# Performance work log

Measured on AMD Instinct MI355X. Metric: run time of the kernel, lower is better.

The kernel has to match this reference:

```python
import jax, jax.numpy as jnp
import numpy as np

P = 1024          # nodes per graph
B = 64            # graphs in batch
N = P * B         # total nodes
E = N * 32        # total edges (avg degree 32)
D_IN = 16         # per-node feature dim (share_obs_dim)
H = 32            # GCN / MLP hidden dim (hardcoded in GNet)
SHARE = 64        # flat share_state dim


def setup_inputs() -> dict:
    key = jax.random.key(0)
    ks = jax.random.split(key, 20)

    x = jax.random.normal(ks[0], (N, D_IN), jnp.float32)
    src = jax.random.randint(ks[1], (E,), 0, N, dtype=jnp.int32)
    # keep edges inside each 1024-node graph block (PyG batched graphs)
    dst = (src // P) * P + jax.random.randint(ks[2], (E,), 0, P, dtype=jnp.int32)
    edge_index = jnp.stack([src, dst])
    value_batch = (jnp.arange(N, dtype=jnp.int32) // P)
    share_state = jax.random.normal(ks[3], (B, SHARE), jnp.float32)

    def lin(k, o, i):
        return jax.random.normal(k, (o, i), jnp.float32) / np.float32(np.sqrt(i))

    return {
        "x": x, "edge_index": edge_index, "value_batch": value_batch,
        "share_state": share_state,
        # value_gnet: GCNConv(D_IN,32), GCNConv(32,32), Linear(32,32), post-pool Linear(32,32)
        "W1": lin(ks[4], H, D_IN), "b1": jnp.zeros((H,), jnp.float32),
        "W2": lin(ks[5], H, H),    "b2": jnp.zeros((H,), jnp.float32),
        "Wl": lin(ks[6], H, H),    "bl": jnp.zeros((H,), jnp.float32),
        "Wp": lin(ks[7], H, H),    "bp": jnp.zeros((H,), jnp.float32),
        # value_net MLP: SHARE->32->32->32
        "Vw1": lin(ks[8], H, SHARE), "Vb1": jnp.zeros((H,), jnp.float32),
        "Vw2": lin(ks[9], H, H),     "Vb2": jnp.zeros((H,), jnp.float32),
        "Vw3": lin(ks[10], H, H),    "Vb3": jnp.zeros((H,), jnp.float32),
        # value_comnet: 64->32->1
        "Cw1": lin(ks[11], H, 2 * H), "Cb1": jnp.zeros((H,), jnp.float32),
        "Cw2": lin(ks[12], 1, H) * np.float32(0.01), "Cb2": jnp.zeros((1,), jnp.float32),
    }


def gcn_conv(x, src, dst, W, b):
    """PyG GCNConv: D^-1/2 (A+I) D^-1/2 X W^T + b (unit edge weights)."""
    n = x.shape[0]
    loop = jnp.arange(n, dtype=src.dtype)
    s = jnp.concatenate([src, loop])
    d = jnp.concatenate([dst, loop])
    deg = jax.ops.segment_sum(jnp.ones(s.shape[0], x.dtype), d, num_segments=n)
    dis = jnp.where(deg > 0, jax.lax.rsqrt(jnp.maximum(deg, 1e-12)), 0.0)
    norm = dis[s] * dis[d]                      # [E+N]
    h = x @ W.T                                  # [N, H] small GEMM first
    out = jax.ops.segment_sum(h[s] * norm[:, None], d, num_segments=n)
    return out + b


def reference(x, edge_index, value_batch, share_state,
              W1, b1, W2, b2, Wl, bl, Wp, bp,
              Vw1, Vb1, Vw2, Vb2, Vw3, Vb3,
              Cw1, Cb1, Cw2, Cb2):
    src, dst = edge_index[0], edge_index[1]
    nb = share_state.shape[0]

    # value_gnet
    h = jnp.tanh(gcn_conv(x, src, dst, W1, b1))
    h = jnp.tanh(gcn_conv(h, src, dst, W2, b2))
    h = jnp.tanh(h @ Wl.T + bl)
    pooled = jax.ops.segment_sum(h, value_batch, num_segments=nb)  # global_add_pool -> [B, 32]
    h1 = pooled @ Wp.T + bp

    # value_net MLP on flat share_state
    h2 = jnp.tanh(share_state @ Vw1.T + Vb1)
    h2 = jnp.tanh(h2 @ Vw2.T + Vb2)
    h2 = h2 @ Vw3.T + Vb3

    # value_comnet
    z = jnp.tanh(jnp.concatenate([h1, h2], axis=-1) @ Cw1.T + Cb1)
    value = z @ Cw2.T + Cb2                      # [B, 1]
    return value
```

## Files before the change

### kernel.cpp

```cpp
#include <hip/hip_runtime.h>
#include <math.h>

#define NNODES 65536
#define NEDGES 2097152
#define PGRAPH 1024
#define NGRAPH 64
#define CAPB   9216
#define CAPQ   9728

#define OFF_GFILL 0u
#define OFF_ARR   1024u
#define OFF_POOL4 1536u
#define OFF_DIS   34304u
#define OFF_EBUF  296448u
#define OFF_H1G   9733632u

__device__ __forceinline__ float ftanh(float x) {
    float e = __expf(2.f * x);
    return 1.f - 2.f * __builtin_amdgcn_rcpf(e + 1.f);
}

__global__ void k_bucket(const int* __restrict__ src, const int* __restrict__ dst,
                         int* __restrict__ gfill, unsigned int* __restrict__ ebuf) {
    __shared__ unsigned int sorted[8192];
    __shared__ int hist[256], lexcl[256], gbase[256], lfill[256];
    __shared__ int wsum[4];
    int t = threadIdx.x;
    hist[t] = 0; lfill[t] = 0;
    __syncthreads();

    const int4* src4 = (const int4*)(src + blockIdx.x * 8192);
    const int4* dst4 = (const int4*)(dst + blockIdx.x * 8192);
    unsigned int pk[32];
    #pragma unroll
    for (int k = 0; k < 8; k++) {
        int4 s4 = src4[k * 256 + t];
        int4 d4 = dst4[k * 256 + t];
        int ss[4] = { s4.x, s4.y, s4.z, s4.w };
        int dd[4] = { d4.x, d4.y, d4.z, d4.w };
        #pragma unroll
        for (int j = 0; j < 4; j++) {
            int g = ss[j] >> 10;
            pk[k * 4 + j] = (unsigned int)((ss[j] & 1023) | ((dd[j] & 1023) << 10) | (g << 20));
            int b = (g << 2) | ((dd[j] >> 8) & 3);
            atomicAdd(&hist[b], 1);
        }
    }
    __syncthreads();

    int h = hist[t];
    int lane = t & 63, wid = t >> 6;
    int xx = h;
    #pragma unroll
    for (int off = 1; off < 64; off <<= 1) {
        int y = __shfl_up(xx, off, 64);
        if (lane >= off) xx += y;
    }
    if (lane == 63) wsum[wid] = xx;
    __syncthreads();
    {
        int pre = 0;
        for (int w = 0; w < wid; w++) pre += wsum[w];
        lexcl[t] = pre + xx - h;
        gbase[t] = atomicAdd(&gfill[t], h);
    }
    __syncthreads();

    #pragma unroll
    for (int k = 0; k < 32; k++) {
        int b = pk[k] >> 18;
        int pos = lexcl[b] + atomicAdd(&lfill[b], 1);
        sorted[pos] = pk[k];
    }
    __syncthreads();
    for (int i = t; i < 8192; i += 256) {
        unsigned int p = sorted[i];
        int b = p >> 18;
        ebuf[(size_t)b * CAPB + gbase[b] + (i - lexcl[b])] = p;
    }
}

__global__ __launch_bounds__(1024, 1) void k_gcn(
        const float* __restrict__ x,
        const float* __restrict__ W1, const float* __restrict__ b1,
        const float* __restrict__ W2, const float* __restrict__ b2,
        const float* __restrict__ Wl, const float* __restrict__ bl,
        const unsigned int* __restrict__ ebuf, const int* __restrict__ gfill,
        float* __restrict__ disg, float* __restrict__ h1g,
        int* __restrict__ arrive, float* __restrict__ pooled4) {
    __shared__ float hsL[1025 * 32];
    __shared__ unsigned short lcsr[CAPQ];
    __shared__ float WlL[32 * 33];
    __shared__ int hist[256], lrow[256], lfill[256];
    __shared__ int wsum[4];
    float4* hsL4 = (float4*)hsL;

    int t = threadIdx.x;
    int g = blockIdx.x & 63, part = blockIdx.x >> 6;
    int bkt = (g << 2) | part;
    int cnt = gfill[bkt];
    const unsigned int* eb = ebuf + (size_t)bkt * CAPB;

    float inr[16];
    {
        const float4* in4 = (const float4*)(x + ((size_t)(g << 10) + t) * 16);
        #pragma unroll
        for (int k = 0; k < 4; k++) {
            float4 v = in4[k];
            inr[4*k] = v.x; inr[4*k+1] = v.y; inr[4*k+2] = v.z; inr[4*k+3] = v.w;
        }
    }

    if (t < 256) hist[t] = 0;
    WlL[(t >> 5) * 33 + (t & 31)] = Wl[t];
    if (t < 32) hsL[1024 * 32 + t] = 0.f;
    __syncthreads();

    for (int i = t; i < cnt; i += 1024) atomicAdd(&hist[(eb[i] >> 10) & 255], 1);
    __syncthreads();

    int dq = 0, r4 = 0;
    if (t < 256) {
        dq = hist[t]; r4 = (dq + 3) & ~3;
        disg[(g << 10) + part * 256 + t] = rsqrtf((float)(dq + 1));
    }
    __syncthreads();
    if (t == 0)
        __hip_atomic_fetch_add(arrive + g, 1, __ATOMIC_RELEASE, __HIP_MEMORY_SCOPE_AGENT);

    int lane = t & 63, wid = t >> 6;
    int xx = r4;
    #pragma unroll
    for (int off = 1; off < 64; off <<= 1) {
        int y = __shfl_up(xx, off, 64);
        if (lane >= off) xx += y;
    }
    if (t < 256 && lane == 63) wsum[wid] = xx;
    __syncthreads();
    if (t < 256) {
        int pre = 0;
        for (int w = 0; w < wid; w++) pre += wsum[w];
        lrow[t] = pre + xx - r4;
        lfill[t] = 0;
    }
    __syncthreads();

    for (int i = t; i < cnt; i += 1024) {
        unsigned int v = eb[i];
        int dl = (v >> 10) & 255;
        int pos = lrow[dl] + atomicAdd(&lfill[dl], 1);
        lcsr[pos] = (unsigned short)(v & 1023);
    }
    if (t < 256) {
        int st = lrow[t];
        for (int i = dq; i < r4; i++) lcsr[st + i] = 1024;
    }

    if (t == 0) {
        while (__hip_atomic_load(arrive + g, __ATOMIC_RELAXED, __HIP_MEMORY_SCOPE_AGENT) < 4) {}
        (void)__hip_atomic_load(arrive + g, __ATOMIC_ACQUIRE, __HIP_MEMORY_SCOPE_AGENT);
    }
    __syncthreads();

    float dis_t = disg[(g << 10) + t];
    int sw = t & 7;

    #pragma unroll
    for (int o4 = 0; o4 < 8; o4++) {
        float r[4];
        #pragma unroll
        for (int j = 0; j < 4; j++) {
            int o = o4 * 4 + j;
            float s = 0.f;
            #pragma unroll
            for (int k = 0; k < 16; k++) s += inr[k] * W1[o * 16 + k];
            r[j] = s * dis_t;
        }
        hsL4[t * 8 + (o4 ^ sw)] = make_float4(r[0], r[1], r[2], r[3]);
    }
    __syncthreads();

    int q = t & 7, grp = t >> 3;
    #pragma unroll
    for (int pass = 0; pass < 2; pass++) {
        int lq = pass * 128 + grp;
        int ln = part * 256 + lq;
        int d = hist[lq];
        float dn = rsqrtf((float)(d + 1));
        int st = lrow[lq];
        float4 acc = hsL4[ln * 8 + (q ^ (ln & 7))];
        const ushort4* c4 = (const ushort4*)(lcsr + st);
        int d4 = (d + 3) >> 2;
        for (int i = 0; i < d4; i++) {
            ushort4 ss = c4[i];
            float4 v0 = hsL4[ss.x * 8 + (q ^ (ss.x & 7))];
            float4 v1 = hsL4[ss.y * 8 + (q ^ (ss.y & 7))];
            float4 v2 = hsL4[ss.z * 8 + (q ^ (ss.z & 7))];
            float4 v3 = hsL4[ss.w * 8 + (q ^ (ss.w & 7))];
            acc.x += (v0.x + v1.x) + (v2.x + v3.x);
            acc.y += (v0.y + v1.y) + (v2.y + v3.y);
            acc.z += (v0.z + v1.z) + (v2.z + v3.z);
            acc.w += (v0.w + v1.w) + (v2.w + v3.w);
        }
        float4 bb = ((const float4*)b1)[q];
        float4 r;
        r.x = ftanh(dn * acc.x + bb.x);
        r.y = ftanh(dn * acc.y + bb.y);
        r.z = ftanh(dn * acc.z + bb.z);
        r.w = ftanh(dn * acc.w + bb.w);
        ((float4*)h1g)[((size_t)(g << 10) + ln) * 8 + q] = r;
    }
    __syncthreads();
    if (t == 0) {
        __hip_atomic_fetch_add(arrive + 64 + g, 1, __ATOMIC_RELEASE, __HIP_MEMORY_SCOPE_AGENT);
        while (__hip_atomic_load(arrive + 64 + g, __ATOMIC_RELAXED, __HIP_MEMORY_SCOPE_AGENT) < 4) {}
        (void)__hip_atomic_load(arrive + 64 + g, __ATOMIC_ACQUIRE, __HIP_MEMORY_SCOPE_AGENT);
    }
    __syncthreads();

    float r2[32];
    {
        const float4* h4 = (const float4*)(h1g + ((size_t)(g << 10) + t) * 32);
        #pragma unroll
        for (int k = 0; k < 8; k++) {
            float4 v = h4[k];
            r2[4*k] = v.x; r2[4*k+1] = v.y; r2[4*k+2] = v.z; r2[4*k+3] = v.w;
        }
    }
    #pragma unroll
    for (int o4 = 0; o4 < 8; o4++) {
        float r[4];
        #pragma unroll
        for (int j = 0; j < 4; j++) {
            int o = o4 * 4 + j;
            float s = 0.f;
            #pragma unroll
            for (int k = 0; k < 32; k++) s += r2[k] * W2[o * 32 + k];
            r[j] = s * dis_t;
        }
        hsL4[t * 8 + (o4 ^ sw)] = make_float4(r[0], r[1], r[2], r[3]);
    }
    __syncthreads();

    float4 racc[2];
    #pragma unroll
    for (int pass = 0; pass < 2; pass++) {
        int lq = pass * 128 + grp;
        int ln = part * 256 + lq;
        int d = hist[lq];
        float dn = rsqrtf((float)(d + 1));
        int st = lrow[lq];
        float4 acc = hsL4[ln * 8 + (q ^ (ln & 7))];
        const ushort4* c4 = (const ushort4*)(lcsr + st);
        int d4 = (d + 3) >> 2;
        for (int i = 0; i < d4; i++) {
            ushort4 ss = c4[i];
            float4 v0 = hsL4[ss.x * 8 + (q ^ (ss.x & 7))];
            float4 v1 = hsL4[ss.y * 8 + (q ^ (ss.y & 7))];
            float4 v2 = hsL4[ss.z * 8 + (q ^ (ss.z & 7))];
            float4 v3 = hsL4[ss.w * 8 + (q ^ (ss.w & 7))];
            acc.x += (v0.x + v1.x) + (v2.x + v3.x);
            acc.y += (v0.y + v1.y) + (v2.y + v3.y);
            acc.z += (v0.z + v1.z) + (v2.z + v3.z);
            acc.w += (v0.w + v1.w) + (v2.w + v3.w);
        }
        float4 bb = ((const float4*)b2)[q];
        float4 r;
        r.x = ftanh(dn * acc.x + bb.x);
        r.y = ftanh(dn * acc.y + bb.y);
        r.z = ftanh(dn * acc.z + bb.z);
        r.w = ftanh(dn * acc.w + bb.w);
        racc[pass] = r;
    }

    __syncthreads();
    #pragma unroll
    for (int pass = 0; pass < 2; pass++) {
        int lnn = pass * 128 + grp;
        hsL4[lnn * 8 + (q ^ (lnn & 7))] = racc[pass];
    }
    __syncthreads();
    int o = t & 31, seg = t >> 5;
    float ps = 0.f;
    #pragma unroll
    for (int j = 0; j < 8; j++) {
        int nl = seg * 8 + j;
        int swn = nl & 7;
        float s = bl[o];
        #pragma unroll
        for (int k = 0; k < 32; k++) {
            float h2v = hsL[nl * 32 + ((((k >> 2) ^ swn) << 2) | (k & 3))];
            s += h2v * WlL[o * 33 + k];
        }
        ps += ftanh(s);
    }
    float* psum = hsL + 8192;
    psum[t] = ps;
    __syncthreads();
    if (t < 32) {
        float tot = 0.f;
        for (int s = 0; s < 32; s++) tot += psum[s * 32 + t];
        pooled4[(g * 4 + part) * 32 + t] = tot;
    }
}

__global__ void k_final(const float* __restrict__ pooled4, const float* __restrict__ share,
                        const float* __restrict__ Wp,  const float* __restrict__ bp,
                        const float* __restrict__ Vw1, const float* __restrict__ Vb1,
                        const float* __restrict__ Vw2, const float* __restrict__ Vb2,
                        const float* __restrict__ Vw3, const float* __restrict__ Vb3,
                        const float* __restrict__ Cw1, const float* __restrict__ Cb1,
                        const float* __restrict__ Cw2, const float* __restrict__ Cb2,
                        float* __restrict__ out) {
    int id = blockIdx.x * 256 + threadIdx.x;
    int b = id >> 5;
    int j = id & 31;
    float p = pooled4[(b * 4 + 0) * 32 + j] + pooled4[(b * 4 + 1) * 32 + j]
            + pooled4[(b * 4 + 2) * 32 + j] + pooled4[(b * 4 + 3) * 32 + j];
    float h1v = bp[j];
    #pragma unroll
    for (int k = 0; k < 32; k++) h1v += Wp[j * 32 + k] * __shfl(p, k, 32);
    float s0 = share[b * 64 + j];
    float s1 = share[b * 64 + 32 + j];
    float t1 = Vb1[j];
    #pragma unroll
    for (int k = 0; k < 32; k++) {
        t1 += Vw1[j * 64 + k] * __shfl(s0, k, 32);
        t1 += Vw1[j * 64 + 32 + k] * __shfl(s1, k, 32);
    }
    t1 = tanhf(t1);
    float t2 = Vb2[j];
    #pragma unroll
    for (int k = 0; k < 32; k++) t2 += Vw2[j * 32 + k] * __shfl(t1, k, 32);
    t2 = tanhf(t2);
    float h2v = Vb3[j];
    #pragma unroll
    for (int k = 0; k < 32; k++) h2v += Vw3[j * 32 + k] * __shfl(t2, k, 32);
    float z = Cb1[j];
    #pragma unroll
    for (int k = 0; k < 32; k++) {
        z += Cw1[j * 64 + k] * __shfl(h1v, k, 32);
        z += Cw1[j * 64 + 32 + k] * __shfl(h2v, k, 32);
    }
    z = tanhf(z);
    float v = Cw2[j] * z;
    v += __shfl_down(v, 16, 32); v += __shfl_down(v, 8, 32);
    v += __shfl_down(v, 4, 32);  v += __shfl_down(v, 2, 32);
    v += __shfl_down(v, 1, 32);
    if (j == 0) out[b] = v + Cb2[0];
}

extern "C" void kernel_launch(void* const* d_in, const int* in_sizes, int n_in,
                              void* d_out, int out_size, void* d_ws, size_t ws_size,
                              hipStream_t stream) {
    const float* x     = (const float*)d_in[0];
    const int*   ei    = (const int*)d_in[1];
    const float* share = (const float*)d_in[3];
    const float* W1 = (const float*)d_in[4];  const float* b1 = (const float*)d_in[5];
    const float* W2 = (const float*)d_in[6];  const float* b2 = (const float*)d_in[7];
    const float* Wl = (const float*)d_in[8];  const float* bl = (const float*)d_in[9];
    const float* Wp = (const float*)d_in[10]; const float* bp = (const float*)d_in[11];
    const float* Vw1 = (const float*)d_in[12]; const float* Vb1 = (const float*)d_in[13];
    const float* Vw2 = (const float*)d_in[14]; const float* Vb2 = (const float*)d_in[15];
    const float* Vw3 = (const float*)d_in[16]; const float* Vb3 = (const float*)d_in[17];
    const float* Cw1 = (const float*)d_in[18]; const float* Cb1 = (const float*)d_in[19];
    const float* Cw2 = (const float*)d_in[20]; const float* Cb2 = (const float*)d_in[21];

    char* ws = (char*)d_ws;
    int*          gfill   = (int*)(ws + OFF_GFILL);
    int*          arrive  = (int*)(ws + OFF_ARR);
    float*        pooled4 = (float*)(ws + OFF_POOL4);
    float*        disg    = (float*)(ws + OFF_DIS);
    unsigned int* ebuf    = (unsigned int*)(ws + OFF_EBUF);
    float*        h1g     = (float*)(ws + OFF_H1G);

    const int* srcp = ei;
    const int* dstp = ei + NEDGES;

    hipMemsetAsync(ws, 0, 1536, stream);

    k_bucket<<<256, 256, 0, stream>>>(srcp, dstp, gfill, ebuf);
    k_gcn<<<256, 1024, 0, stream>>>(x, W1, b1, W2, b2, Wl, bl,
                                    ebuf, gfill, disg, h1g, arrive, pooled4);
    k_final<<<8, 256, 0, stream>>>(pooled4, share, Wp, bp, Vw1, Vb1, Vw2, Vb2,
                                   Vw3, Vb3, Cw1, Cb1, Cw2, Cb2, (float*)d_out);
}
```

Baseline: 179.2 us.

## Split GCN node transforms across partition blocks and exchange half-precision features

Before, every block of a graph recomputed the X·W1 and H·W2 transforms for all 1024 nodes and exchanged fp32 layer-1 outputs through global memory. Now each of the four blocks computes the transform only for its own 256 nodes, stores the degree-scaled result as fp16 both in shared memory and in a global exchange buffer, and then copies the other 768 rows in after the inter-block barrier. The shared-memory gather during aggregation reads half-precision rows, which halves LDS traffic per neighbour. Layer outputs are kept in a transposed shared buffer so the next matmul and the final linear+pool can read them directly. This cuts redundant arithmetic and halves the feature storage, at the cost of fp16 rounding on the messages and an extra global round trip for the transformed features.

```diff
diff --git a/kernel.cpp b/kernel.cpp
--- a/kernel.cpp
+++ b/kernel.cpp
@@ -1,4 +1,5 @@
 #include <hip/hip_runtime.h>
+#include <hip/hip_fp16.h>
 #include <math.h>
 
 #define NNODES 65536
@@ -11,13 +12,20 @@
 #define OFF_GFILL 0u
 #define OFF_ARR   1024u
 #define OFF_POOL4 1536u
-#define OFF_DIS   34304u
-#define OFF_EBUF  296448u
-#define OFF_H1G   9733632u
+#define OFF_EBUF  34304u
+#define OFF_HS1   9471488u
+#define OFF_HS2   13665792u
 
 __device__ __forceinline__ float ftanh(float x) {
     float e = __expf(2.f * x);
     return 1.f - 2.f * __builtin_amdgcn_rcpf(e + 1.f);
+}
+
+__device__ __forceinline__ float4 ld4h(const unsigned int* hs, int r, int q) {
+    uint2 u = *(const uint2*)(hs + r * 16 + ((q ^ (r & 7)) << 1));
+    float2 fa = __half22float2(*(const __half2*)&u.x);
+    float2 fb = __half22float2(*(const __half2*)&u.y);
+    return make_float4(fa.x, fa.y, fb.x, fb.y);
 }
 
 __global__ void k_bucket(const int* __restrict__ src, const int* __restrict__ dst,
@@ -86,14 +94,15 @@
         const float* __restrict__ W2, const float* __restrict__ b2,
         const float* __restrict__ Wl, const float* __restrict__ bl,
         const unsigned int* __restrict__ ebuf, const int* __restrict__ gfill,
-        float* __restrict__ disg, float* __restrict__ h1g,
+        unsigned int* __restrict__ hs1g, unsigned int* __restrict__ hs2g,
         int* __restrict__ arrive, float* __restrict__ pooled4) {
-    __shared__ float hsL[1025 * 32];
+    __shared__ unsigned int hsLh[1025 * 16];
     __shared__ unsigned short lcsr[CAPQ];
-    __shared__ float WlL[32 * 33];
+    __shared__ float h1T[32 * 257];
+    __shared__ float W2L[32 * 33];
+    __shared__ float disL[256];
     __shared__ int hist[256], lrow[256], lfill[256];
     __shared__ int wsum[4];
-    float4* hsL4 = (float4*)hsL;
 
     int t = threadIdx.x;
     int g = blockIdx.x & 63, part = blockIdx.x >> 6;
@@ -101,33 +110,54 @@
     int cnt = gfill[bkt];
     const unsigned int* eb = ebuf + (size_t)bkt * CAPB;
 
-    float inr[16];
+    int nl = t >> 2, og = t & 3;
+    float4 v4 = ((const float4*)(x + ((size_t)((g << 10) + (part << 8) + nl)) * 16))[og];
+
+    if (t < 256) hist[t] = 0;
+    W2L[(t >> 5) * 33 + (t & 31)] = W2[t];
+    if (t < 16) hsLh[1024 * 16 + t] = 0u;
+    __syncthreads();
+
+    for (int i = t; i < cnt; i += 1024) atomicAdd(&hist[(eb[i] >> 10) & 255], 1);
+    __syncthreads();
+    if (t < 256) disL[t] = rsqrtf((float)(hist[t] + 1));
+    __syncthreads();
+
+    float xk[16];
+    #pragma unroll
+    for (int d = 0; d < 4; d++) {
+        xk[4*d+0] = __shfl(v4.x, d, 4);
+        xk[4*d+1] = __shfl(v4.y, d, 4);
+        xk[4*d+2] = __shfl(v4.z, d, 4);
+        xk[4*d+3] = __shfl(v4.w, d, 4);
+    }
+    int ln = (part << 8) + nl;
+    int s7own = ln & 7;
     {
-        const float4* in4 = (const float4*)(x + ((size_t)(g << 10) + t) * 16);
-        #pragma unroll
-        for (int k = 0; k < 4; k++) {
-            float4 v = in4[k];
-            inr[4*k] = v.x; inr[4*k+1] = v.y; inr[4*k+2] = v.z; inr[4*k+3] = v.w;
+        float dnl = disL[nl];
+        unsigned int uo[4];
+        #pragma unroll
+        for (int p2 = 0; p2 < 4; p2++) {
+            int o0 = og * 8 + p2 * 2;
+            float s0 = 0.f, s1 = 0.f;
+            #pragma unroll
+            for (int k = 0; k < 16; k++) {
+                s0 += xk[k] * W1[o0 * 16 + k];
+                s1 += xk[k] * W1[o0 * 16 + 16 + k];
+            }
+            __half2 hh = __floats2half2_rn(s0 * dnl, s1 * dnl);
+            uo[p2] = *(unsigned int*)&hh;
         }
-    }
-
-    if (t < 256) hist[t] = 0;
-    WlL[(t >> 5) * 33 + (t & 31)] = Wl[t];
-    if (t < 32) hsL[1024 * 32 + t] = 0.f;
-    __syncthreads();
-
-    for (int i = t; i < cnt; i += 1024) atomicAdd(&hist[(eb[i] >> 10) & 255], 1);
-    __syncthreads();
-
-    int dq = 0, r4 = 0;
-    if (t < 256) {
-        dq = hist[t]; r4 = (dq + 3) & ~3;
-        disg[(g << 10) + part * 256 + t] = rsqrtf((float)(dq + 1));
+        ((uint4*)hs1g)[((size_t)(g << 10) + ln) * 4 + og] = make_uint4(uo[0], uo[1], uo[2], uo[3]);
+        *(uint2*)&hsLh[ln * 16 + ((( (2*og)     ^ s7own)) << 1)] = make_uint2(uo[0], uo[1]);
+        *(uint2*)&hsLh[ln * 16 + ((( (2*og + 1) ^ s7own)) << 1)] = make_uint2(uo[2], uo[3]);
     }
     __syncthreads();
     if (t == 0)
         __hip_atomic_fetch_add(arrive + g, 1, __ATOMIC_RELEASE, __HIP_MEMORY_SCOPE_AGENT);
 
+    int dq = 0, r4 = 0;
+    if (t < 256) { dq = hist[t]; r4 = (dq + 3) & ~3; }
     int lane = t & 63, wid = t >> 6;
     int xx = r4;
     #pragma unroll
@@ -144,7 +174,6 @@
         lfill[t] = 0;
     }
     __syncthreads();
-
     for (int i = t; i < cnt; i += 1024) {
         unsigned int v = eb[i];
         int dl = (v >> 10) & 255;
@@ -162,21 +191,16 @@
     }
     __syncthreads();
 
-    float dis_t = disg[(g << 10) + t];
-    int sw = t & 7;
-
-    #pragma unroll
-    for (int o4 = 0; o4 < 8; o4++) {
-        float r[4];
-        #pragma unroll
-        for (int j = 0; j < 4; j++) {
-            int o = o4 * 4 + j;
-            float s = 0.f;
-            #pragma unroll
-            for (int k = 0; k < 16; k++) s += inr[k] * W1[o * 16 + k];
-            r[j] = s * dis_t;
-        }
-        hsL4[t * 8 + (o4 ^ sw)] = make_float4(r[0], r[1], r[2], r[3]);
+    if (t < 768) {
+        int r = (((part + 1) << 8) + t) & 1023;
+        const uint4* s4 = (const uint4*)hs1g + ((size_t)(g << 10) + r) * 4;
+        uint4 ua = s4[0], ub = s4[1], uc = s4[2], ud = s4[3];
+        unsigned int u[16] = { ua.x, ua.y, ua.z, ua.w, ub.x, ub.y, ub.z, ub.w,
+                               uc.x, uc.y, uc.z, uc.w, ud.x, ud.y, ud.z, ud.w };
+        int s7 = r & 7;
+        #pragma unroll
+        for (int p = 0; p < 8; p++)
+            *(uint2*)&hsLh[r * 16 + ((p ^ s7) << 1)] = make_uint2(u[2*p], u[2*p+1]);
     }
     __syncthreads();
 
@@ -184,31 +208,53 @@
     #pragma unroll
     for (int pass = 0; pass < 2; pass++) {
         int lq = pass * 128 + grp;
-        int ln = part * 256 + lq;
+        int lnq = (part << 8) + lq;
         int d = hist[lq];
-        float dn = rsqrtf((float)(d + 1));
+        float dn = disL[lq];
         int st = lrow[lq];
-        float4 acc = hsL4[ln * 8 + (q ^ (ln & 7))];
+        float4 acc = ld4h(hsLh, lnq, q);
         const ushort4* c4 = (const ushort4*)(lcsr + st);
         int d4 = (d + 3) >> 2;
         for (int i = 0; i < d4; i++) {
             ushort4 ss = c4[i];
-            float4 v0 = hsL4[ss.x * 8 + (q ^ (ss.x & 7))];
-            float4 v1 = hsL4[ss.y * 8 + (q ^ (ss.y & 7))];
-            float4 v2 = hsL4[ss.z * 8 + (q ^ (ss.z & 7))];
-            float4 v3 = hsL4[ss.w * 8 + (q ^ (ss.w & 7))];
+            float4 v0 = ld4h(hsLh, ss.x, q);
+            float4 v1 = ld4h(hsLh, ss.y, q);
+            float4 v2 = ld4h(hsLh, ss.z, q);
+            float4 v3 = ld4h(hsLh, ss.w, q);
             acc.x += (v0.x + v1.x) + (v2.x + v3.x);
             acc.y += (v0.y + v1.y) + (v2.y + v3.y);
             acc.z += (v0.z + v1.z) + (v2.z + v3.z);
             acc.w += (v0.w + v1.w) + (v2.w + v3.w);
         }
         float4 bb = ((const float4*)b1)[q];
-        float4 r;
-        r.x = ftanh(dn * acc.x + bb.x);
-        r.y = ftanh(dn * acc.y + bb.y);
-        r.z = ftanh(dn * acc.z + bb.z);
-        r.w = ftanh(dn * acc.w + bb.w);
-        ((float4*)h1g)[((size_t)(g << 10) + ln) * 8 + q] = r;
+        h1T[(4*q+0)*257 + lq] = ftanh(dn * acc.x + bb.x);
+        h1T[(4*q+1)*257 + lq] = ftanh(dn * acc.y + bb.y);
+        h1T[(4*q+2)*257 + lq] = ftanh(dn * acc.z + bb.z);
+        h1T[(4*q+3)*257 + lq] = ftanh(dn * acc.w + bb.w);
+    }
+    __syncthreads();
+
+    {
+        float hk[32];
+        #pragma unroll
+        for (int k = 0; k < 32; k++) hk[k] = h1T[k*257 + nl];
+        float dnl = disL[nl];
+        unsigned int vo[4];
+        #pragma unroll
+        for (int p2 = 0; p2 < 4; p2++) {
+            int o0 = og * 8 + p2 * 2;
+            float s0 = 0.f, s1 = 0.f;
+            #pragma unroll
+            for (int k = 0; k < 32; k++) {
+                s0 += hk[k] * W2L[o0*33 + k];
+                s1 += hk[k] * W2L[(o0+1)*33 + k];
+            }
+            __half2 hh = __floats2half2_rn(s0 * dnl, s1 * dnl);
+            vo[p2] = *(unsigned int*)&hh;
+        }
+        ((uint4*)hs2g)[((size_t)(g << 10) + ln) * 4 + og] = make_uint4(vo[0], vo[1], vo[2], vo[3]);
+        *(uint2*)&hsLh[ln * 16 + ((( (2*og)     ^ s7own)) << 1)] = make_uint2(vo[0], vo[1]);
+        *(uint2*)&hsLh[ln * 16 + ((( (2*og + 1) ^ s7own)) << 1)] = make_uint2(vo[2], vo[3]);
     }
     __syncthreads();
     if (t == 0) {
@@ -218,88 +264,68 @@
     }
     __syncthreads();
 
-    float r2[32];
-    {
-        const float4* h4 = (const float4*)(h1g + ((size_t)(g << 10) + t) * 32);
-        #pragma unroll
-        for (int k = 0; k < 8; k++) {
-            float4 v = h4[k];
-            r2[4*k] = v.x; r2[4*k+1] = v.y; r2[4*k+2] = v.z; r2[4*k+3] = v.w;
-        }
-    }
-    #pragma unroll
-    for (int o4 = 0; o4 < 8; o4++) {
-        float r[4];
-        #pragma unroll
-        for (int j = 0; j < 4; j++) {
-            int o = o4 * 4 + j;
-            float s = 0.f;
-            #pragma unroll
-            for (int k = 0; k < 32; k++) s += r2[k] * W2[o * 32 + k];
-            r[j] = s * dis_t;
-        }
-        hsL4[t * 8 + (o4 ^ sw)] = make_float4(r[0], r[1], r[2], r[3]);
-    }
-    __syncthreads();
-
-    float4 racc[2];
+    if (t < 768) {
+        int r = (((part + 1) << 8) + t) & 1023;
+        const uint4* s4 = (const uint4*)hs2g + ((size_t)(g << 10) + r) * 4;
+        uint4 ua = s4[0], ub = s4[1], uc = s4[2], ud = s4[3];
+        unsigned int u[16] = { ua.x, ua.y, ua.z, ua.w, ub.x, ub.y, ub.z, ub.w,
+                               uc.x, uc.y, uc.z, uc.w, ud.x, ud.y, ud.z, ud.w };
+        int s7 = r & 7;
+        #pragma unroll
+        for (int p = 0; p < 8; p++)
+            *(uint2*)&hsLh[r * 16 + ((p ^ s7) << 1)] = make_uint2(u[2*p], u[2*p+1]);
+    }
+    __syncthreads();
+
     #pragma unroll
     for (int pass = 0; pass < 2; pass++) {
         int lq = pass * 128 + grp;
-        int ln = part * 256 + lq;
+        int lnq = (part << 8) + lq;
         int d = hist[lq];
-        float dn = rsqrtf((float)(d + 1));
+        float dn = disL[lq];
         int st = lrow[lq];
-        float4 acc = hsL4[ln * 8 + (q ^ (ln & 7))];
+        float4 acc = ld4h(hsLh, lnq, q);
         const ushort4* c4 = (const ushort4*)(lcsr + st);
         int d4 = (d + 3) >> 2;
         for (int i = 0; i < d4; i++) {
             ushort4 ss = c4[i];
-            float4 v0 = hsL4[ss.x * 8 + (q ^ (ss.x & 7))];
-            float4 v1 = hsL4[ss.y * 8 + (q ^ (ss.y & 7))];
-            float4 v2 = hsL4[ss.z * 8 + (q ^ (ss.z & 7))];
-            float4 v3 = hsL4[ss.w * 8 + (q ^ (ss.w & 7))];
+            float4 v0 = ld4h(hsLh, ss.x, q);
+            float4 v1 = ld4h(hsLh, ss.y, q);
+            float4 v2 = ld4h(hsLh, ss.z, q);
+            float4 v3 = ld4h(hsLh, ss.w, q);
             acc.x += (v0.x + v1.x) + (v2.x + v3.x);
             acc.y += (v0.y + v1.y) + (v2.y + v3.y);
             acc.z += (v0.z + v1.z) + (v2.z + v3.z);
             acc.w += (v0.w + v1.w) + (v2.w + v3.w);
         }
         float4 bb = ((const float4*)b2)[q];
-        float4 r;
-        r.x = ftanh(dn * acc.x + bb.x);
-        r.y = ftanh(dn * acc.y + bb.y);
-        r.z = ftanh(dn * acc.z + bb.z);
-        r.w = ftanh(dn * acc.w + bb.w);
-        racc[pass] = r;
-    }
-
-    __syncthreads();
-    #pragma unroll
-    for (int pass = 0; pass < 2; pass++) {
-        int lnn = pass * 128 + grp;
-        hsL4[lnn * 8 + (q ^ (lnn & 7))] = racc[pass];
-    }
-    __syncthreads();
+        h1T[(4*q+0)*257 + lq] = ftanh(dn * acc.x + bb.x);
+        h1T[(4*q+1)*257 + lq] = ftanh(dn * acc.y + bb.y);
+        h1T[(4*q+2)*257 + lq] = ftanh(dn * acc.z + bb.z);
+        h1T[(4*q+3)*257 + lq] = ftanh(dn * acc.w + bb.w);
+    }
+    __syncthreads();
+
     int o = t & 31, seg = t >> 5;
+    float wlr[32];
+    #pragma unroll
+    for (int k = 0; k < 32; k++) wlr[k] = Wl[o*32 + k];
+    float blv = bl[o];
     float ps = 0.f;
     #pragma unroll
     for (int j = 0; j < 8; j++) {
-        int nl = seg * 8 + j;
-        int swn = nl & 7;
-        float s = bl[o];
-        #pragma unroll
-        for (int k = 0; k < 32; k++) {
-            float h2v = hsL[nl * 32 + ((((k >> 2) ^ swn) << 2) | (k & 3))];
-            s += h2v * WlL[o * 33 + k];
-        }
+        int nn = seg * 8 + j;
+        float s = blv;
+        #pragma unroll
+        for (int k = 0; k < 32; k++) s += h1T[k*257 + nn] * wlr[k];
         ps += ftanh(s);
     }
-    float* psum = hsL + 8192;
+    float* psum = (float*)hsLh;
     psum[t] = ps;
     __syncthreads();
     if (t < 32) {
         float tot = 0.f;
-        for (int s = 0; s < 32; s++) tot += psum[s * 32 + t];
+        for (int s2 = 0; s2 < 32; s2++) tot += psum[s2 * 32 + t];
         pooled4[(g * 4 + part) * 32 + t] = tot;
     }
 }
@@ -370,9 +396,9 @@
     int*          gfill   = (int*)(ws + OFF_GFILL);
     int*          arrive  = (int*)(ws + OFF_ARR);
     float*        pooled4 = (float*)(ws + OFF_POOL4);
-    float*        disg    = (float*)(ws + OFF_DIS);
     unsigned int* ebuf    = (unsigned int*)(ws + OFF_EBUF);
-    float*        h1g     = (float*)(ws + OFF_H1G);
+    unsigned int* hs1g    = (unsigned int*)(ws + OFF_HS1);
+    unsigned int* hs2g    = (unsigned int*)(ws + OFF_HS2);
 
     const int* srcp = ei;
     const int* dstp = ei + NEDGES;
@@ -381,7 +407,7 @@
 
     k_bucket<<<256, 256, 0, stream>>>(srcp, dstp, gfill, ebuf);
     k_gcn<<<256, 1024, 0, stream>>>(x, W1, b1, W2, b2, Wl, bl,
-                                    ebuf, gfill, disg, h1g, arrive, pooled4);
+                                    ebuf, gfill, hs1g, hs2g, arrive, pooled4);
     k_final<<<8, 256, 0, stream>>>(pooled4, share, Wp, bp, Vw1, Vb1, Vw2, Vb2,
                                    Vw3, Vb3, Cw1, Cb1, Cw2, Cb2, (float*)d_out);
 }
```

Result: slower. 208.8 us (+16.5%).

## Process one graph per block with fp16 LDS features and fused final MLP

Applied to the files above, without the earlier changes.

Switches from four blocks per graph, which synchronised through global atomics and wrote intermediate h1 to global memory, to a single 1024-thread block per graph. Node features are held in LDS as fp16 so the whole graph fits, the second GCN layer reads h1 straight from LDS, and the final MLP is fused into the same kernel. This removes the cross-block spin waits, the global round trip and one launch. In exchange only 64 blocks run, each thread does four times the aggregation work, and fp16 storage adds rounding error.

```diff
diff --git a/kernel.cpp b/kernel.cpp
--- a/kernel.cpp
+++ b/kernel.cpp
@@ -1,32 +1,40 @@
 #include <hip/hip_runtime.h>
+#include <hip/hip_fp16.h>
 #include <math.h>
 
 #define NNODES 65536
 #define NEDGES 2097152
 #define PGRAPH 1024
 #define NGRAPH 64
-#define CAPB   9216
-#define CAPQ   9728
+#define CAPE   34560
+#define CAPG   37888
 
 #define OFF_GFILL 0u
-#define OFF_ARR   1024u
-#define OFF_POOL4 1536u
-#define OFF_DIS   34304u
-#define OFF_EBUF  296448u
-#define OFF_H1G   9733632u
+#define OFF_EBUF  8192u
 
 __device__ __forceinline__ float ftanh(float x) {
     float e = __expf(2.f * x);
     return 1.f - 2.f * __builtin_amdgcn_rcpf(e + 1.f);
 }
 
+__device__ __forceinline__ float4 ld4h(const unsigned int* hs, int r, int q) {
+    uint2 u = *(const uint2*)(hs + r * 16 + ((q ^ (r & 7)) << 1));
+    float2 fa = __half22float2(*(const __half2*)&u.x);
+    float2 fb = __half22float2(*(const __half2*)&u.y);
+    return make_float4(fa.x, fa.y, fb.x, fb.y);
+}
+__device__ __forceinline__ uint2 pk4h(float a, float b, float c, float d) {
+    __half2 h0 = __floats2half2_rn(a, b);
+    __half2 h1 = __floats2half2_rn(c, d);
+    return make_uint2(*(unsigned int*)&h0, *(unsigned int*)&h1);
+}
+
 __global__ void k_bucket(const int* __restrict__ src, const int* __restrict__ dst,
                          int* __restrict__ gfill, unsigned int* __restrict__ ebuf) {
     __shared__ unsigned int sorted[8192];
-    __shared__ int hist[256], lexcl[256], gbase[256], lfill[256];
-    __shared__ int wsum[4];
+    __shared__ int hist[64], lexcl[64], gbase[64], lfill[64];
     int t = threadIdx.x;
-    hist[t] = 0; lfill[t] = 0;
+    if (t < 64) { hist[t] = 0; lfill[t] = 0; }
     __syncthreads();
 
     const int4* src4 = (const int4*)(src + blockIdx.x * 8192);
@@ -42,41 +50,33 @@
         for (int j = 0; j < 4; j++) {
             int g = ss[j] >> 10;
             pk[k * 4 + j] = (unsigned int)((ss[j] & 1023) | ((dd[j] & 1023) << 10) | (g << 20));
-            int b = (g << 2) | ((dd[j] >> 8) & 3);
-            atomicAdd(&hist[b], 1);
-        }
-    }
-    __syncthreads();
-
-    int h = hist[t];
-    int lane = t & 63, wid = t >> 6;
-    int xx = h;
-    #pragma unroll
-    for (int off = 1; off < 64; off <<= 1) {
-        int y = __shfl_up(xx, off, 64);
-        if (lane >= off) xx += y;
-    }
-    if (lane == 63) wsum[wid] = xx;
-    __syncthreads();
-    {
-        int pre = 0;
-        for (int w = 0; w < wid; w++) pre += wsum[w];
-        lexcl[t] = pre + xx - h;
-        gbase[t] = atomicAdd(&gfill[t], h);
-    }
-    __syncthreads();
-
+            atomicAdd(&hist[g], 1);
+        }
+    }
+    __syncthreads();
+    if (t < 64) {
+        int h = hist[t];
+        int x = h;
+        #pragma unroll
+        for (int off = 1; off < 64; off <<= 1) {
+            int y = __shfl_up(x, off, 64);
+            if (t >= off) x += y;
+        }
+        lexcl[t] = x - h;
+        gbase[t] = atomicAdd(&gfill[t << 5], h);
+    }
+    __syncthreads();
     #pragma unroll
     for (int k = 0; k < 32; k++) {
-        int b = pk[k] >> 18;
-        int pos = lexcl[b] + atomicAdd(&lfill[b], 1);
+        int g = pk[k] >> 20;
+        int pos = lexcl[g] + atomicAdd(&lfill[g], 1);
         sorted[pos] = pk[k];
     }
     __syncthreads();
     for (int i = t; i < 8192; i += 256) {
         unsigned int p = sorted[i];
-        int b = p >> 18;
-        ebuf[(size_t)b * CAPB + gbase[b] + (i - lexcl[b])] = p;
+        int g = p >> 20;
+        ebuf[(size_t)g * CAPE + gbase[g] + (i - lexcl[g])] = p;
     }
 }
 
@@ -85,25 +85,29 @@
         const float* __restrict__ W1, const float* __restrict__ b1,
         const float* __restrict__ W2, const float* __restrict__ b2,
         const float* __restrict__ Wl, const float* __restrict__ bl,
+        const float* __restrict__ Wp, const float* __restrict__ bp,
+        const float* __restrict__ Vw1, const float* __restrict__ Vb1,
+        const float* __restrict__ Vw2, const float* __restrict__ Vb2,
+        const float* __restrict__ Vw3, const float* __restrict__ Vb3,
+        const float* __restrict__ Cw1, const float* __restrict__ Cb1,
+        const float* __restrict__ Cw2, const float* __restrict__ Cb2,
+        const float* __restrict__ share,
         const unsigned int* __restrict__ ebuf, const int* __restrict__ gfill,
-        float* __restrict__ disg, float* __restrict__ h1g,
-        int* __restrict__ arrive, float* __restrict__ pooled4) {
-    __shared__ float hsL[1025 * 32];
-    __shared__ unsigned short lcsr[CAPQ];
-    __shared__ float WlL[32 * 33];
-    __shared__ int hist[256], lrow[256], lfill[256];
-    __shared__ int wsum[4];
-    float4* hsL4 = (float4*)hsL;
+        float* __restrict__ out) {
+    __shared__ unsigned int hsLh[1025 * 16];
+    __shared__ __align__(16) unsigned short lcsr[CAPG];
+    __shared__ float disL[1024];
+    __shared__ int hist[1024], lrow[1024], lfill[1024];
+    __shared__ int wsum[16];
 
     int t = threadIdx.x;
-    int g = blockIdx.x & 63, part = blockIdx.x >> 6;
-    int bkt = (g << 2) | part;
-    int cnt = gfill[bkt];
-    const unsigned int* eb = ebuf + (size_t)bkt * CAPB;
+    int g = blockIdx.x;
+    int cnt = gfill[g << 5];
+    const unsigned int* eb = ebuf + (size_t)g * CAPE;
 
     float inr[16];
     {
-        const float4* in4 = (const float4*)(x + ((size_t)(g << 10) + t) * 16);
+        const float4* in4 = (const float4*)(x + ((size_t)((g << 10) + t)) * 16);
         #pragma unroll
         for (int k = 0; k < 4; k++) {
             float4 v = in4[k];
@@ -111,22 +115,16 @@
         }
     }
 
-    if (t < 256) hist[t] = 0;
-    WlL[(t >> 5) * 33 + (t & 31)] = Wl[t];
-    if (t < 32) hsL[1024 * 32 + t] = 0.f;
-    __syncthreads();
-
-    for (int i = t; i < cnt; i += 1024) atomicAdd(&hist[(eb[i] >> 10) & 255], 1);
-    __syncthreads();
-
-    int dq = 0, r4 = 0;
-    if (t < 256) {
-        dq = hist[t]; r4 = (dq + 3) & ~3;
-        disg[(g << 10) + part * 256 + t] = rsqrtf((float)(dq + 1));
-    }
-    __syncthreads();
-    if (t == 0)
-        __hip_atomic_fetch_add(arrive + g, 1, __ATOMIC_RELEASE, __HIP_MEMORY_SCOPE_AGENT);
+    hist[t] = 0;
+    if (t < 16) hsLh[1024 * 16 + t] = 0u;
+    __syncthreads();
+
+    for (int i = t; i < cnt; i += 1024) atomicAdd(&hist[(eb[i] >> 10) & 1023], 1);
+    __syncthreads();
+
+    int dq = hist[t];
+    int r4 = (dq + 3) & ~3;
+    disL[t] = rsqrtf((float)(dq + 1));
 
     int lane = t & 63, wid = t >> 6;
     int xx = r4;
@@ -135,9 +133,9 @@
         int y = __shfl_up(xx, off, 64);
         if (lane >= off) xx += y;
     }
-    if (t < 256 && lane == 63) wsum[wid] = xx;
-    __syncthreads();
-    if (t < 256) {
+    if (lane == 63) wsum[wid] = xx;
+    __syncthreads();
+    {
         int pre = 0;
         for (int w = 0; w < wid; w++) pre += wsum[w];
         lrow[t] = pre + xx - r4;
@@ -147,24 +145,17 @@
 
     for (int i = t; i < cnt; i += 1024) {
         unsigned int v = eb[i];
-        int dl = (v >> 10) & 255;
+        int dl = (v >> 10) & 1023;
         int pos = lrow[dl] + atomicAdd(&lfill[dl], 1);
         lcsr[pos] = (unsigned short)(v & 1023);
     }
-    if (t < 256) {
+    {
         int st = lrow[t];
         for (int i = dq; i < r4; i++) lcsr[st + i] = 1024;
     }
 
-    if (t == 0) {
-        while (__hip_atomic_load(arrive + g, __ATOMIC_RELAXED, __HIP_MEMORY_SCOPE_AGENT) < 4) {}
-        (void)__hip_atomic_load(arrive + g, __ATOMIC_ACQUIRE, __HIP_MEMORY_SCOPE_AGENT);
-    }
-    __syncthreads();
-
-    float dis_t = disg[(g << 10) + t];
+    float dn_t = disL[t];
     int sw = t & 7;
-
     #pragma unroll
     for (int o4 = 0; o4 < 8; o4++) {
         float r[4];
@@ -174,180 +165,167 @@
             float s = 0.f;
             #pragma unroll
             for (int k = 0; k < 16; k++) s += inr[k] * W1[o * 16 + k];
-            r[j] = s * dis_t;
-        }
-        hsL4[t * 8 + (o4 ^ sw)] = make_float4(r[0], r[1], r[2], r[3]);
+            r[j] = s * dn_t;
+        }
+        *(uint2*)&hsLh[t * 16 + ((o4 ^ sw) << 1)] = pk4h(r[0], r[1], r[2], r[3]);
     }
     __syncthreads();
 
     int q = t & 7, grp = t >> 3;
-    #pragma unroll
-    for (int pass = 0; pass < 2; pass++) {
-        int lq = pass * 128 + grp;
-        int ln = part * 256 + lq;
-        int d = hist[lq];
-        float dn = rsqrtf((float)(d + 1));
-        int st = lrow[lq];
-        float4 acc = hsL4[ln * 8 + (q ^ (ln & 7))];
+    float4 hacc[8];
+    #pragma unroll
+    for (int p = 0; p < 8; p++) {
+        int node = p * 128 + grp;
+        int d = hist[node];
+        float dn = disL[node];
+        int st = lrow[node];
+        float4 acc = ld4h(hsLh, node, q);
         const ushort4* c4 = (const ushort4*)(lcsr + st);
         int d4 = (d + 3) >> 2;
         for (int i = 0; i < d4; i++) {
             ushort4 ss = c4[i];
-            float4 v0 = hsL4[ss.x * 8 + (q ^ (ss.x & 7))];
-            float4 v1 = hsL4[ss.y * 8 + (q ^ (ss.y & 7))];
-            float4 v2 = hsL4[ss.z * 8 + (q ^ (ss.z & 7))];
-            float4 v3 = hsL4[ss.w * 8 + (q ^ (ss.w & 7))];
+            float4 v0 = ld4h(hsLh, ss.x, q);
+            float4 v1 = ld4h(hsLh, ss.y, q);
+            float4 v2 = ld4h(hsLh, ss.z, q);
+            float4 v3 = ld4h(hsLh, ss.w, q);
             acc.x += (v0.x + v1.x) + (v2.x + v3.x);
             acc.y += (v0.y + v1.y) + (v2.y + v3.y);
             acc.z += (v0.z + v1.z) + (v2.z + v3.z);
             acc.w += (v0.w + v1.w) + (v2.w + v3.w);
         }
         float4 bb = ((const float4*)b1)[q];
-        float4 r;
-        r.x = ftanh(dn * acc.x + bb.x);
-        r.y = ftanh(dn * acc.y + bb.y);
-        r.z = ftanh(dn * acc.z + bb.z);
-        r.w = ftanh(dn * acc.w + bb.w);
-        ((float4*)h1g)[((size_t)(g << 10) + ln) * 8 + q] = r;
-    }
-    __syncthreads();
-    if (t == 0) {
-        __hip_atomic_fetch_add(arrive + 64 + g, 1, __ATOMIC_RELEASE, __HIP_MEMORY_SCOPE_AGENT);
-        while (__hip_atomic_load(arrive + 64 + g, __ATOMIC_RELAXED, __HIP_MEMORY_SCOPE_AGENT) < 4) {}
-        (void)__hip_atomic_load(arrive + 64 + g, __ATOMIC_ACQUIRE, __HIP_MEMORY_SCOPE_AGENT);
-    }
-    __syncthreads();
-
-    float r2[32];
+        hacc[p] = make_float4(ftanh(dn * acc.x + bb.x), ftanh(dn * acc.y + bb.y),
+                              ftanh(dn * acc.z + bb.z), ftanh(dn * acc.w + bb.w));
+    }
+    __syncthreads();
+
+    #pragma unroll
+    for (int p = 0; p < 8; p++) {
+        int node = p * 128 + grp;
+        *(uint2*)&hsLh[node * 16 + ((q ^ (node & 7)) << 1)] =
+            pk4h(hacc[p].x, hacc[p].y, hacc[p].z, hacc[p].w);
+    }
+    __syncthreads();
+
     {
-        const float4* h4 = (const float4*)(h1g + ((size_t)(g << 10) + t) * 32);
-        #pragma unroll
-        for (int k = 0; k < 8; k++) {
-            float4 v = h4[k];
-            r2[4*k] = v.x; r2[4*k+1] = v.y; r2[4*k+2] = v.z; r2[4*k+3] = v.w;
-        }
-    }
-    #pragma unroll
-    for (int o4 = 0; o4 < 8; o4++) {
-        float r[4];
-        #pragma unroll
-        for (int j = 0; j < 4; j++) {
-            int o = o4 * 4 + j;
-            float s = 0.f;
+        float hk[32];
+        #pragma unroll
+        for (int p2 = 0; p2 < 8; p2++) {
+            uint2 u = *(const uint2*)&hsLh[t * 16 + ((p2 ^ sw) << 1)];
+            float2 fa = __half22float2(*(const __half2*)&u.x);
+            float2 fb = __half22float2(*(const __half2*)&u.y);
+            hk[4*p2] = fa.x; hk[4*p2+1] = fa.y; hk[4*p2+2] = fb.x; hk[4*p2+3] = fb.y;
+        }
+        #pragma unroll
+        for (int o4 = 0; o4 < 8; o4++) {
+            float r[4];
             #pragma unroll
-            for (int k = 0; k < 32; k++) s += r2[k] * W2[o * 32 + k];
-            r[j] = s * dis_t;
-        }
-        hsL4[t * 8 + (o4 ^ sw)] = make_float4(r[0], r[1], r[2], r[3]);
-    }
-    __syncthreads();
-
-    float4 racc[2];
-    #pragma unroll
-    for (int pass = 0; pass < 2; pass++) {
-        int lq = pass * 128 + grp;
-        int ln = part * 256 + lq;
-        int d = hist[lq];
-        float dn = rsqrtf((float)(d + 1));
-        int st = lrow[lq];
-        float4 acc = hsL4[ln * 8 + (q ^ (ln & 7))];
+            for (int j = 0; j < 4; j++) {
+                int o = o4 * 4 + j;
+                float s = 0.f;
+                #pragma unroll
+                for (int k = 0; k < 32; k++) s += hk[k] * W2[o * 32 + k];
+                r[j] = s * dn_t;
+            }
+            *(uint2*)&hsLh[t * 16 + ((o4 ^ sw) << 1)] = pk4h(r[0], r[1], r[2], r[3]);
+        }
+    }
+    __syncthreads();
+
+    float4 h2acc[8];
+    #pragma unroll
+    for (int p = 0; p < 8; p++) {
+        int node = p * 128 + grp;
+        int d = hist[node];
+        float dn = disL[node];
+        int st = lrow[node];
+        float4 acc = ld4h(hsLh, node, q);
         const ushort4* c4 = (const ushort4*)(lcsr + st);
         int d4 = (d + 3) >> 2;
         for (int i = 0; i < d4; i++) {
             ushort4 ss = c4[i];
-            float4 v0 = hsL4[ss.x * 8 + (q ^ (ss.x & 7))];
-            float4 v1 = hsL4[ss.y * 8 + (q ^ (ss.y & 7))];
-            float4 v2 = hsL4[ss.z * 8 + (q ^ (ss.z & 7))];
-            float4 v3 = hsL4[ss.w * 8 + (q ^ (ss.w & 7))];
+            float4 v0 = ld4h(hsLh, ss.x, q);
+            float4 v1 = ld4h(hsLh, ss.y, q);
+            float4 v2 = ld4h(hsLh, ss.z, q);
+            float4 v3 = ld4h(hsLh, ss.w, q);
             acc.x += (v0.x + v1.x) + (v2.x + v3.x);
             acc.y += (v0.y + v1.y) + (v2.y + v3.y);
             acc.z += (v0.z + v1.z) + (v2.z + v3.z);
             acc.w += (v0.w + v1.w) + (v2.w + v3.w);
         }
         float4 bb = ((const float4*)b2)[q];
-        float4 r;
-        r.x = ftanh(dn * acc.x + bb.x);
-        r.y = ftanh(dn * acc.y + bb.y);
-        r.z = ftanh(dn * acc.z + bb.z);
-        r.w = ftanh(dn * acc.w + bb.w);
-        racc[pass] = r;
-    }
-
-    __syncthreads();
-    #pragma unroll
-    for (int pass = 0; pass < 2; pass++) {
-        int lnn = pass * 128 + grp;
-        hsL4[lnn * 8 + (q ^ (lnn & 7))] = racc[pass];
-    }
-    __syncthreads();
+        h2acc[p] = make_float4(ftanh(dn * acc.x + bb.x), ftanh(dn * acc.y + bb.y),
+                               ftanh(dn * acc.z + bb.z), ftanh(dn * acc.w + bb.w));
+    }
+    __syncthreads();
+
+    #pragma unroll
+    for (int p = 0; p < 8; p++) {
+        int node = p * 128 + grp;
+        *(uint2*)&hsLh[node * 16 + ((q ^ (node & 7)) << 1)] =
+            pk4h(h2acc[p].x, h2acc[p].y, h2acc[p].z, h2acc[p].w);
+    }
+    __syncthreads();
+
     int o = t & 31, seg = t >> 5;
+    float wlr[32];
+    #pragma unroll
+    for (int k = 0; k < 32; k++) wlr[k] = Wl[o * 32 + k];
+    float blv = bl[o];
     float ps = 0.f;
-    #pragma unroll
-    for (int j = 0; j < 8; j++) {
-        int nl = seg * 8 + j;
-        int swn = nl & 7;
-        float s = bl[o];
+    for (int j = 0; j < 32; j++) {
+        int nn = seg * 32 + j;
+        int s7 = nn & 7;
+        float s = blv;
+        #pragma unroll
+        for (int p2 = 0; p2 < 8; p2++) {
+            uint2 u = *(const uint2*)&hsLh[nn * 16 + ((p2 ^ s7) << 1)];
+            float2 fa = __half22float2(*(const __half2*)&u.x);
+            float2 fb = __half22float2(*(const __half2*)&u.y);
+            s += fa.x * wlr[4*p2] + fa.y * wlr[4*p2+1] + fb.x * wlr[4*p2+2] + fb.y * wlr[4*p2+3];
+        }
+        ps += ftanh(s);
+    }
+    float* psum = (float*)lrow;
+    psum[t] = ps;
+    __syncthreads();
+
+    if (t < 32) {
+        int j = t;
+        float p = 0.f;
+        for (int s2 = 0; s2 < 32; s2++) p += psum[s2 * 32 + j];
+        float h1v = bp[j];
+        #pragma unroll
+        for (int k = 0; k < 32; k++) h1v += Wp[j * 32 + k] * __shfl(p, k, 32);
+        float s0 = share[g * 64 + j];
+        float s1 = share[g * 64 + 32 + j];
+        float t1 = Vb1[j];
         #pragma unroll
         for (int k = 0; k < 32; k++) {
-            float h2v = hsL[nl * 32 + ((((k >> 2) ^ swn) << 2) | (k & 3))];
-            s += h2v * WlL[o * 33 + k];
-        }
-        ps += ftanh(s);
-    }
-    float* psum = hsL + 8192;
-    psum[t] = ps;
-    __syncthreads();
-    if (t < 32) {
-        float tot = 0.f;
-        for (int s = 0; s < 32; s++) tot += psum[s * 32 + t];
-        pooled4[(g * 4 + part) * 32 + t] = tot;
-    }
-}
-
-__global__ void k_final(const float* __restrict__ pooled4, const float* __restrict__ share,
-                        const float* __restrict__ Wp,  const float* __restrict__ bp,
-                        const float* __restrict__ Vw1, const float* __restrict__ Vb1,
-                        const float* __restrict__ Vw2, const float* __restrict__ Vb2,
-                        const float* __restrict__ Vw3, const float* __restrict__ Vb3,
-                        const float* __restrict__ Cw1, const float* __restrict__ Cb1,
-                        const float* __restrict__ Cw2, const float* __restrict__ Cb2,
-                        float* __restrict__ out) {
-    int id = blockIdx.x * 256 + threadIdx.x;
-    int b = id >> 5;
-    int j = id & 31;
-    float p = pooled4[(b * 4 + 0) * 32 + j] + pooled4[(b * 4 + 1) * 32 + j]
-            + pooled4[(b * 4 + 2) * 32 + j] + pooled4[(b * 4 + 3) * 32 + j];
-    float h1v = bp[j];
-    #pragma unroll
-    for (int k = 0; k < 32; k++) h1v += Wp[j * 32 + k] * __shfl(p, k, 32);
-    float s0 = share[b * 64 + j];
-    float s1 = share[b * 64 + 32 + j];
-    float t1 = Vb1[j];
-    #pragma unroll
-    for (int k = 0; k < 32; k++) {
-        t1 += Vw1[j * 64 + k] * __shfl(s0, k, 32);
-        t1 += Vw1[j * 64 + 32 + k] * __shfl(s1, k, 32);
-    }
-    t1 = tanhf(t1);
-    float t2 = Vb2[j];
-    #pragma unroll
-    for (int k = 0; k < 32; k++) t2 += Vw2[j * 32 + k] * __shfl(t1, k, 32);
-    t2 = tanhf(t2);
-    float h2v = Vb3[j];
-    #pragma unroll
-    for (int k = 0; k < 32; k++) h2v += Vw3[j * 32 + k] * __shfl(t2, k, 32);
-    float z = Cb1[j];
-    #pragma unroll
-    for (int k = 0; k < 32; k++) {
-        z += Cw1[j * 64 + k] * __shfl(h1v, k, 32);
-        z += Cw1[j * 64 + 32 + k] * __shfl(h2v, k, 32);
-    }
-    z = tanhf(z);
-    float v = Cw2[j] * z;
-    v += __shfl_down(v, 16, 32); v += __shfl_down(v, 8, 32);
-    v += __shfl_down(v, 4, 32);  v += __shfl_down(v, 2, 32);
-    v += __shfl_down(v, 1, 32);
-    if (j == 0) out[b] = v + Cb2[0];
+            t1 += Vw1[j * 64 + k] * __shfl(s0, k, 32);
+            t1 += Vw1[j * 64 + 32 + k] * __shfl(s1, k, 32);
+        }
+        t1 = tanhf(t1);
+        float t2 = Vb2[j];
+        #pragma unroll
+        for (int k = 0; k < 32; k++) t2 += Vw2[j * 32 + k] * __shfl(t1, k, 32);
+        t2 = tanhf(t2);
+        float h2v = Vb3[j];
+        #pragma unroll
+        for (int k = 0; k < 32; k++) h2v += Vw3[j * 32 + k] * __shfl(t2, k, 32);
+        float z = Cb1[j];
+        #pragma unroll
+        for (int k = 0; k < 32; k++) {
+            z += Cw1[j * 64 + k] * __shfl(h1v, k, 32);
+            z += Cw1[j * 64 + 32 + k] * __shfl(h2v, k, 32);
+        }
+        z = tanhf(z);
+        float v = Cw2[j] * z;
+        v += __shfl_down(v, 16, 32); v += __shfl_down(v, 8, 32);
+        v += __shfl_down(v, 4, 32);  v += __shfl_down(v, 2, 32);
+        v += __shfl_down(v, 1, 32);
+        if (j == 0) out[g] = v + Cb2[0];
+    }
 }
 
 extern "C" void kernel_launch(void* const* d_in, const int* in_sizes, int n_in,
@@ -367,21 +345,17 @@
     const float* Cw2 = (const float*)d_in[20]; const float* Cb2 = (const float*)d_in[21];
 
     char* ws = (char*)d_ws;
-    int*          gfill   = (int*)(ws + OFF_GFILL);
-    int*          arrive  = (int*)(ws + OFF_ARR);
-    float*        pooled4 = (float*)(ws + OFF_POOL4);
-    float*        disg    = (float*)(ws + OFF_DIS);
-    unsigned int* ebuf    = (unsigned int*)(ws + OFF_EBUF);
-    float*        h1g     = (float*)(ws + OFF_H1G);
+    int*          gfill = (int*)(ws + OFF_GFILL);
+    unsigned int* ebuf  = (unsigned int*)(ws + OFF_EBUF);
 
     const int* srcp = ei;
     const int* dstp = ei + NEDGES;
 
-    hipMemsetAsync(ws, 0, 1536, stream);
+    hipMemsetAsync(gfill, 0, 8192, stream);
 
     k_bucket<<<256, 256, 0, stream>>>(srcp, dstp, gfill, ebuf);
-    k_gcn<<<256, 1024, 0, stream>>>(x, W1, b1, W2, b2, Wl, bl,
-                                    ebuf, gfill, disg, h1g, arrive, pooled4);
-    k_final<<<8, 256, 0, stream>>>(pooled4, share, Wp, bp, Vw1, Vb1, Vw2, Vb2,
-                                   Vw3, Vb3, Cw1, Cb1, Cw2, Cb2, (float*)d_out);
-}
+    k_gcn<<<64, 1024, 0, stream>>>(x, W1, b1, W2, b2, Wl, bl, Wp, bp,
+                                   Vw1, Vb1, Vw2, Vb2, Vw3, Vb3,
+                                   Cw1, Cb1, Cw2, Cb2, share,
+                                   ebuf, gfill, (float*)d_out);
+}
```

After: 240.6 us. +34.2%, slower.
